# Kernel optimization log

Measured on AMD Instinct MI355X. Metric: run time of the kernel, lower is better.

## Reference

```python
import jax, jax.numpy as jnp
import numpy as np

EMBED_DIM = 2048
NUM_HEADS = 32
NUM_KV_GROUPS = 8
HEAD_DIM = EMBED_DIM // NUM_HEADS  # 64
KV_DIM = HEAD_DIM * NUM_KV_GROUPS  # 512
SCALE = HEAD_DIM ** -0.5


def setup_inputs() -> dict:
    key = jax.random.key(0)
    ks = jax.random.split(key, 11)
    B, T, C = 2, 2048, EMBED_DIM
    s = C ** -0.5
    return {
        "query": jax.random.normal(ks[0], (B, T, C), jnp.float32),
        "key": jax.random.normal(ks[1], (B, T, C), jnp.float32),
        "value": jax.random.normal(ks[2], (B, T, C), jnp.float32),
        "q_w": jax.random.normal(ks[3], (C, C), jnp.float32) * s,
        "q_b": jnp.zeros((C,), jnp.float32),
        "k_w": jax.random.normal(ks[4], (KV_DIM, C), jnp.float32) * s,
        "k_b": jnp.zeros((KV_DIM,), jnp.float32),
        "v_w": jax.random.normal(ks[5], (KV_DIM, C), jnp.float32) * s,
        "v_b": jnp.zeros((KV_DIM,), jnp.float32),
        "o_w": jax.random.normal(ks[6], (C, C), jnp.float32) * s,
        "o_b": jnp.zeros((C,), jnp.float32),
    }


def reference(query, key, value, q_w, q_b, k_w, k_b, v_w, v_b, o_w, o_b):
    B, T, C = query.shape
    n_rep = NUM_HEADS // NUM_KV_GROUPS
    # projections (torch Linear: x @ W.T + b)
    q = (query @ q_w.T + q_b).reshape(B, T, NUM_HEADS, HEAD_DIM)
    k = (key @ k_w.T + k_b).reshape(B, T, NUM_KV_GROUPS, HEAD_DIM)
    v = (value @ v_w.T + v_b).reshape(B, T, NUM_KV_GROUPS, HEAD_DIM)
    # GQA: expand KV groups to match query heads (repeat_interleave on head dim)
    k = jnp.repeat(k, n_rep, axis=2)  # (B, T, H, hd)
    v = jnp.repeat(v, n_rep, axis=2)
    q = jnp.transpose(q, (0, 2, 1, 3)) * SCALE  # (B, H, T, hd)
    k = jnp.transpose(k, (0, 2, 1, 3))
    v = jnp.transpose(v, (0, 2, 1, 3))
    scores = jnp.einsum("bhqd,bhkd->bhqk", q, k)  # (B, H, T, T)
    attn = jax.nn.softmax(scores.astype(jnp.float32), axis=-1).astype(query.dtype)
    out = jnp.einsum("bhqk,bhkd->bhqd", attn, v)  # (B, H, T, hd)
    out = jnp.transpose(out, (0, 2, 1, 3)).reshape(B, T, C)
    return out @ o_w.T + o_b
```

## Files before the change

kernel.cpp:

```cpp
#include <hip/hip_runtime.h>
#include <stdint.h>
#include <stddef.h>

using short8 = __attribute__((ext_vector_type(8))) short;
using short4v = __attribute__((ext_vector_type(4))) short;
using f32x4  = __attribute__((ext_vector_type(4))) float;
using f32x16 = __attribute__((ext_vector_type(16))) float;
using bf16x8 = __attribute__((ext_vector_type(8))) __bf16;

#define DEVI __device__ __forceinline__

DEVI short bf16r(float f) {
  union { float f; uint32_t u; } x; x.f = f;
  uint32_t r = x.u + 0x7FFFu + ((x.u >> 16) & 1u);
  return (short)(r >> 16);
}

DEVI f32x4 mfma16(short8 a, short8 b, f32x4 c) {
  return __builtin_amdgcn_mfma_f32_16x16x32_bf16(
      __builtin_bit_cast(bf16x8, a), __builtin_bit_cast(bf16x8, b), c, 0, 0, 0);
}

DEVI f32x16 mfma32(short8 a, short8 b, f32x16 c) {
  return __builtin_amdgcn_mfma_f32_32x32x16_bf16(
      __builtin_bit_cast(bf16x8, a), __builtin_bit_cast(bf16x8, b), c, 0, 0, 0);
}

DEVI void gload_lds16(const void* g, void* l) {
  __builtin_amdgcn_global_load_lds(
      (const void __attribute__((address_space(1)))*)g,
      (void __attribute__((address_space(3)))*)l,
      16, 0, 0);
}

DEVI float fexp2(float x) {
  float r;
  asm("v_exp_f32 %0, %1" : "=v"(r) : "v"(x));
  return r;
}

DEVI unsigned cvtpk(float a, float b) {
  unsigned r;
  asm("v_cvt_pk_bf16_f32 %0, %1, %2" : "=v"(r) : "v"(a), "v"(b));
  return r;
}

__global__ void k_cvt2(const float* __restrict__ s0, short* __restrict__ d0,
                       const float* __restrict__ s1, short* __restrict__ d1, int n4) {
  const float* s = blockIdx.z ? s1 : s0;
  short* d = blockIdx.z ? d1 : d0;
  int i = blockIdx.x * blockDim.x + threadIdx.x;
  if (i < n4) {
    f32x4 v = reinterpret_cast<const f32x4*>(s)[i];
    short4v o;
    o[0] = bf16r(v[0]); o[1] = bf16r(v[1]); o[2] = bf16r(v[2]); o[3] = bf16r(v[3]);
    reinterpret_cast<short4v*>(d)[i] = o;
  }
}

__global__ void k_cvt(const float* __restrict__ src, short* __restrict__ dst, int n4) {
  int i = blockIdx.x * blockDim.x + threadIdx.x;
  if (i < n4) {
    f32x4 v = reinterpret_cast<const f32x4*>(src)[i];
    short4v o;
    o[0] = bf16r(v[0]); o[1] = bf16r(v[1]); o[2] = bf16r(v[2]); o[3] = bf16r(v[3]);
    reinterpret_cast<short4v*>(dst)[i] = o;
  }
}

template<bool OUT_F32, bool DUAL>
__global__ __launch_bounds__(256) void k_gemm(
    const short* __restrict__ Aw, const short* __restrict__ Bw,
    const float* __restrict__ bias, void* __restrict__ Cp,
    const short* __restrict__ Aw2, const short* __restrict__ Bw2,
    const float* __restrict__ bias2, void* __restrict__ Cp2,
    int M, int N, int K, float alpha)
{
  if constexpr (DUAL) {
    if (blockIdx.z) { Aw = Aw2; Bw = Bw2; bias = bias2; Cp = Cp2; }
  }
  __shared__ short As[2][128 * 64];
  __shared__ short Bs[2][128 * 64];
  const int t = threadIdx.x;
  const int lane = t & 63;
  const int wid = t >> 6;
  const int wr = wid >> 1, wc = wid & 1;
  const int bm = blockIdx.y * 128;
  const int bn = blockIdx.x * 128;

  f32x4 acc[4][4];
  #pragma unroll
  for (int i = 0; i < 4; ++i)
    #pragma unroll
    for (int j = 0; j < 4; ++j) acc[i][j] = f32x4{0.f, 0.f, 0.f, 0.f};

  const int nt = K >> 6;

  auto stage = [&](const short* G, short (&buf)[128 * 64], int k0) {
    #pragma unroll
    for (int i = 0; i < 4; ++i) {
      int lin = t * 16 + i * 4096;
      int a = lin ^ (((lin >> 7) & 7) << 4);
      int row = a >> 7;
      int col = (a & 127) >> 1;
      const short* g = G + (size_t)row * K + k0 + col;
      gload_lds16(g, (char*)(&buf[0]) + (wid << 10) + (i << 12));
    }
  };

  stage(Aw + (size_t)bm * K, As[0], 0);
  stage(Bw + (size_t)bn * K, Bs[0], 0);
  __syncthreads();

  int cur = 0;
  for (int kt = 0; kt < nt; ++kt) {
    const bool pf = (kt + 1 < nt);
    if (pf) {
      stage(Aw + (size_t)bm * K, As[cur ^ 1], (kt + 1) << 6);
      stage(Bw + (size_t)bn * K, Bs[cur ^ 1], (kt + 1) << 6);
    }
    #pragma unroll
    for (int kk = 0; kk < 2; ++kk) {
      const int kb = (kk * 32 + ((lane >> 4) << 3)) << 1;
      short8 af[4], bfr[4];
      #pragma unroll
      for (int i = 0; i < 4; ++i) {
        int row = wr * 64 + i * 16 + (lane & 15);
        int byte = ((row << 7) + kb) ^ ((row & 7) << 4);
        af[i] = *reinterpret_cast<const short8*>((const char*)(&As[cur][0]) + byte);
      }
      #pragma unroll
      for (int j = 0; j < 4; ++j) {
        int row = wc * 64 + j * 16 + (lane & 15);
        int byte = ((row << 7) + kb) ^ ((row & 7) << 4);
        bfr[j] = *reinterpret_cast<const short8*>((const char*)(&Bs[cur][0]) + byte);
      }
      __builtin_amdgcn_s_setprio(1);
      #pragma unroll
      for (int i = 0; i < 4; ++i)
        #pragma unroll
        for (int j = 0; j < 4; ++j)
          acc[i][j] = mfma16(af[i], bfr[j], acc[i][j]);
      __builtin_amdgcn_s_setprio(0);
    }
    __syncthreads();
    cur ^= 1;
  }

  #pragma unroll
  for (int j = 0; j < 4; ++j) {
    int col = bn + wc * 64 + j * 16 + (lane & 15);
    float bv = bias[col];
    #pragma unroll
    for (int i = 0; i < 4; ++i) {
      int row0 = bm + wr * 64 + i * 16 + ((lane >> 4) << 2);
      #pragma unroll
      for (int r = 0; r < 4; ++r) {
        float v = (acc[i][j][r] + bv) * alpha;
        if constexpr (OUT_F32)
          ((float*)Cp)[(size_t)(row0 + r) * N + col] = v;
        else
          ((short*)Cp)[(size_t)(row0 + r) * N + col] = bf16r(v);
      }
    }
  }
}

__global__ __launch_bounds__(512) void k_attn(
    const short* __restrict__ Q, const short* __restrict__ Kg,
    const short* __restrict__ Vg, short* __restrict__ Op)
{
  constexpr int T = 2048;
  constexpr int NT = T / 64;

  const int orig = blockIdx.x;
  const int wgid = (orig & 7) * 64 + (orig >> 3);
  const int bh = wgid >> 3;
  const int qb = wgid & 7;
  const int b = bh >> 5, h = bh & 31;
  const int g = h >> 2;
  const int q0 = qb * 256;

  const int t = threadIdx.x;
  const int lane = t & 63;
  const int wid = t >> 6;
  const int lo = lane & 31;
  const int hi = lane >> 5;

  __shared__ alignas(16) union {
    struct {
      short Kl[2][64 * 64];
      short Vt[2][64 * 72];
    } s;
    short Ol[8][32 * 72];
  } sm;

  const size_t qrow = (size_t)(b * T + q0 + wid * 32 + lo);
  short8 qf[4];
  #pragma unroll
  for (int s = 0; s < 4; ++s)
    qf[s] = *reinterpret_cast<const short8*>(Q + qrow * 2048 + h * 64 + s * 16 + hi * 8);

  f32x16 o0, o1;
  #pragma unroll
  for (int r = 0; r < 16; ++r) { o0[r] = 0.f; o1[r] = 0.f; }
  float m = -10000.f, l = 0.f;

  const short* Kbase = Kg + (size_t)(b * T) * 512 + g * 64;
  const short* Vbase = Vg + (size_t)(b * T) * 512 + g * 64;

  auto stageK = [&](int buf, int k0) {
    int lin = t * 16;
    int a = lin ^ (((lin >> 7) & 7) << 4);
    int row = a >> 7;
    int col = (a & 127) >> 1;
    gload_lds16(Kbase + (size_t)(k0 + row) * 512 + col,
                (char*)(&sm.s.Kl[buf][0]) + (wid << 10));
  };
  short8 vreg;
  auto loadV = [&](int k0) {
    vreg = *reinterpret_cast<const short8*>(
        Vbase + (size_t)(k0 + lane) * 512 + wid * 8);
  };
  auto writeV = [&](int buf) {
    #pragma unroll
    for (int e = 0; e < 8; ++e)
      sm.s.Vt[buf][(wid * 8 + e) * 72 + lane] = vreg[e];
  };

  stageK(0, 0);
  loadV(0);
  writeV(0);
  __syncthreads();

  int cur = 0;
  for (int kt = 0; kt < NT; ++kt) {
    const bool pf = (kt + 1 < NT);
    if (pf) { stageK(cur ^ 1, (kt + 1) * 64); loadV((kt + 1) * 64); }

    short8 kf[2][4];
    #pragma unroll
    for (int tt = 0; tt < 2; ++tt)
      #pragma unroll
      for (int s = 0; s < 4; ++s) {
        int row = tt * 32 + lo;
        int byte = ((row << 7) + (s << 5) + (hi << 4)) ^ ((row & 7) << 4);
        kf[tt][s] = *reinterpret_cast<const short8*>((const char*)(&sm.s.Kl[cur][0]) + byte);
      }
    f32x16 st0, st1;
    #pragma unroll
    for (int r = 0; r < 16; ++r) { st0[r] = 0.f; st1[r] = 0.f; }
    #pragma unroll
    for (int s = 0; s < 4; ++s) {
      st0 = mfma32(kf[0][s], qf[s], st0);
      st1 = mfma32(kf[1][s], qf[s], st1);
    }

    float mx = st0[0];
    #pragma unroll
    for (int r = 1; r < 16; ++r) mx = fmaxf(mx, st0[r]);
    #pragma unroll
    for (int r = 0; r < 16; ++r) mx = fmaxf(mx, st1[r]);
    mx = fmaxf(mx, __shfl_xor(mx, 32));
    if (!__all(mx - m <= 8.0f)) {
      float mn = fmaxf(m, mx);
      float sc = fexp2(m - mn);
      m = mn; l *= sc;
      o0 = o0 * sc; o1 = o1 * sc;
    }
    float ssum = 0.f;
    #pragma unroll
    for (int r = 0; r < 16; ++r) { float e = fexp2(st0[r] - m); st0[r] = e; ssum += e; }
    #pragma unroll
    for (int r = 0; r < 16; ++r) { float e = fexp2(st1[r] - m); st1[r] = e; ssum += e; }
    ssum += __shfl_xor(ssum, 32);
    l += ssum;

    short8 pb[4];
    #pragma unroll
    for (int tt = 0; tt < 2; ++tt) {
      const f32x16& sv = tt ? st1 : st0;
      #pragma unroll
      for (int half = 0; half < 2; ++half) {
        unsigned x1 = cvtpk(sv[half * 8 + 0], sv[half * 8 + 1]);
        unsigned x2 = cvtpk(sv[half * 8 + 2], sv[half * 8 + 3]);
        unsigned x3 = cvtpk(sv[half * 8 + 4], sv[half * 8 + 5]);
        unsigned x4 = cvtpk(sv[half * 8 + 6], sv[half * 8 + 7]);
        unsigned y1 = __shfl_xor(x1, 32);
        unsigned y2 = __shfl_xor(x2, 32);
        unsigned y3 = __shfl_xor(x3, 32);
        unsigned y4 = __shfl_xor(x4, 32);
        union { unsigned u[4]; short8 s8; } p;
        p.u[0] = hi ? y3 : x1;
        p.u[1] = hi ? y4 : x2;
        p.u[2] = hi ? x3 : y1;
        p.u[3] = hi ? x4 : y2;
        pb[tt * 2 + half] = p.s8;
      }
    }

    #pragma unroll
    for (int ks = 0; ks < 4; ++ks) {
      {
        int byte = (lo * 144) + (ks << 5) + (hi << 4);
        short8 va = *reinterpret_cast<const short8*>((const char*)(&sm.s.Vt[cur][0]) + byte);
        o0 = mfma32(va, pb[ks], o0);
      }
      {
        int byte = ((32 + lo) * 144) + (ks << 5) + (hi << 4);
        short8 va = *reinterpret_cast<const short8*>((const char*)(&sm.s.Vt[cur][0]) + byte);
        o1 = mfma32(va, pb[ks], o1);
      }
    }

    if (pf) writeV(cur ^ 1);
    __syncthreads();
    cur ^= 1;
  }

  float inv = 1.0f / l;
  #pragma unroll
  for (int dt = 0; dt < 2; ++dt) {
    const f32x16& ov = dt ? o1 : o0;
    #pragma unroll
    for (int r = 0; r < 16; r += 2) {
      unsigned d2 = cvtpk(ov[r] * inv, ov[r + 1] * inv);
      int dpos = dt * 32 + (r & 3) + 8 * (r >> 2) + 4 * hi;
      *reinterpret_cast<unsigned*>((char*)(&sm.Ol[wid][0]) + (lo * 72 + dpos) * 2) = d2;
    }
  }
  __syncthreads();
  #pragma unroll
  for (int i = 0; i < 4; ++i) {
    int c = hi * 4 + i;
    short8 v = *reinterpret_cast<const short8*>((const char*)(&sm.Ol[wid][0]) + lo * 144 + c * 16);
    *reinterpret_cast<short8*>(Op + qrow * 2048 + h * 64 + c * 8) = v;
  }
}

extern "C" void kernel_launch(void* const* d_in, const int* in_sizes, int n_in,
                              void* d_out, int out_size, void* d_ws, size_t ws_size,
                              hipStream_t stream)
{
  const float* query = (const float*)d_in[0];
  const float* key   = (const float*)d_in[1];
  const float* value = (const float*)d_in[2];
  const float* q_w   = (const float*)d_in[3];
  const float* q_b   = (const float*)d_in[4];
  const float* k_w   = (const float*)d_in[5];
  const float* k_b   = (const float*)d_in[6];
  const float* v_w   = (const float*)d_in[7];
  const float* v_b   = (const float*)d_in[8];
  const float* o_w   = (const float*)d_in[9];
  const float* o_b   = (const float*)d_in[10];
  float* out = (float*)d_out;

  char* ws = (char*)d_ws;
  short* q_wb = (short*)(ws);
  short* k_wb = (short*)(ws + 8388608);
  short* v_wb = (short*)(ws + 10485760);
  short* o_wb = (short*)(ws + 12582912);
  short* R1   = (short*)(ws + 20971520);
  short* R2   = (short*)(ws + 37748736);
  short* Kp   = (short*)(ws + 54525952);
  short* Vp   = (short*)(ws + 58720256);

  const float ALPHA_Q = 0.125f * 1.4426950408889634f;

  k_cvt2<<<dim3(4096, 1, 2), 256, 0, stream>>>(q_w, q_wb, o_w, o_wb, 1048576);
  k_cvt2<<<dim3(1024, 1, 2), 256, 0, stream>>>(k_w, k_wb, v_w, v_wb, 262144);
  k_cvt2<<<dim3(8192, 1, 2), 256, 0, stream>>>(key, R1, value, R2, 2097152);

  k_gemm<false, true><<<dim3(4, 32, 2), 256, 0, stream>>>(
      R1, k_wb, k_b, Kp, R2, v_wb, v_b, Vp, 4096, 512, 2048, 1.0f);

  k_cvt<<<8192, 256, 0, stream>>>(query, R1, 2097152);

  k_gemm<false, false><<<dim3(16, 32), 256, 0, stream>>>(
      R1, q_wb, q_b, R2, nullptr, nullptr, nullptr, nullptr, 4096, 2048, 2048, ALPHA_Q);

  k_attn<<<dim3(512), dim3(512), 0, stream>>>(R2, Kp, Vp, R1);

  k_gemm<true, false><<<dim3(16, 32), 256, 0, stream>>>(
      R1, o_wb, o_b, out, nullptr, nullptr, nullptr, nullptr, 4096, 2048, 2048, 1.0f);
}
```

Measured before the change: 257.6 us.

## Software-pipeline attention loop: overlap next QK^T with current PV, triple-buffer V

After: 263.1 us. 2.1% more time.

```diff
diff --git a/kernel.cpp b/kernel.cpp
--- a/kernel.cpp
+++ b/kernel.cpp
@@ -166,7 +166,7 @@
   }
 }
 
-__global__ __launch_bounds__(512) void k_attn(
+__global__ __launch_bounds__(512, 4) void k_attn(
     const short* __restrict__ Q, const short* __restrict__ Kg,
     const short* __restrict__ Vg, short* __restrict__ Op)
 {
@@ -190,7 +190,7 @@
   __shared__ alignas(16) union {
     struct {
       short Kl[2][64 * 64];
-      short Vt[2][64 * 72];
+      short Vt[3][64 * 72];
     } s;
     short Ol[8][32 * 72];
   } sm;
@@ -228,34 +228,38 @@
       sm.s.Vt[buf][(wid * 8 + e) * 72 + lane] = vreg[e];
   };
 
-  stageK(0, 0);
-  loadV(0);
-  writeV(0);
-  __syncthreads();
-
-  int cur = 0;
-  for (int kt = 0; kt < NT; ++kt) {
-    const bool pf = (kt + 1 < NT);
-    if (pf) { stageK(cur ^ 1, (kt + 1) * 64); loadV((kt + 1) * 64); }
-
-    short8 kf[2][4];
-    #pragma unroll
-    for (int tt = 0; tt < 2; ++tt)
+  f32x16 st0, st1;
+  short8 pb[4];
+
+  auto qkt = [&](int kbuf) {
+    const char* base = (const char*)(&sm.s.Kl[kbuf][0]);
+    #pragma unroll
+    for (int r = 0; r < 16; ++r) { st0[r] = 0.f; st1[r] = 0.f; }
+    {
+      short8 kf[4];
       #pragma unroll
       for (int s = 0; s < 4; ++s) {
-        int row = tt * 32 + lo;
+        int row = lo;
         int byte = ((row << 7) + (s << 5) + (hi << 4)) ^ ((row & 7) << 4);
-        kf[tt][s] = *reinterpret_cast<const short8*>((const char*)(&sm.s.Kl[cur][0]) + byte);
-      }
-    f32x16 st0, st1;
-    #pragma unroll
-    for (int r = 0; r < 16; ++r) { st0[r] = 0.f; st1[r] = 0.f; }
-    #pragma unroll
-    for (int s = 0; s < 4; ++s) {
-      st0 = mfma32(kf[0][s], qf[s], st0);
-      st1 = mfma32(kf[1][s], qf[s], st1);
-    }
-
+        kf[s] = *reinterpret_cast<const short8*>(base + byte);
+      }
+      #pragma unroll
+      for (int s = 0; s < 4; ++s) st0 = mfma32(kf[s], qf[s], st0);
+    }
+    {
+      short8 kf[4];
+      #pragma unroll
+      for (int s = 0; s < 4; ++s) {
+        int row = 32 + lo;
+        int byte = ((row << 7) + (s << 5) + (hi << 4)) ^ ((row & 7) << 4);
+        kf[s] = *reinterpret_cast<const short8*>(base + byte);
+      }
+      #pragma unroll
+      for (int s = 0; s < 4; ++s) st1 = mfma32(kf[s], qf[s], st1);
+    }
+  };
+
+  auto softmax_pack = [&]() {
     float mx = st0[0];
     #pragma unroll
     for (int r = 1; r < 16; ++r) mx = fmaxf(mx, st0[r]);
@@ -276,7 +280,6 @@
     ssum += __shfl_xor(ssum, 32);
     l += ssum;
 
-    short8 pb[4];
     #pragma unroll
     for (int tt = 0; tt < 2; ++tt) {
       const f32x16& sv = tt ? st1 : st0;
@@ -298,25 +301,48 @@
         pb[tt * 2 + half] = p.s8;
       }
     }
-
+  };
+
+  auto pv = [&](int vbuf) {
+    const char* base = (const char*)(&sm.s.Vt[vbuf][0]);
     #pragma unroll
     for (int ks = 0; ks < 4; ++ks) {
       {
         int byte = (lo * 144) + (ks << 5) + (hi << 4);
-        short8 va = *reinterpret_cast<const short8*>((const char*)(&sm.s.Vt[cur][0]) + byte);
+        short8 va = *reinterpret_cast<const short8*>(base + byte);
         o0 = mfma32(va, pb[ks], o0);
       }
       {
         int byte = ((32 + lo) * 144) + (ks << 5) + (hi << 4);
-        short8 va = *reinterpret_cast<const short8*>((const char*)(&sm.s.Vt[cur][0]) + byte);
+        short8 va = *reinterpret_cast<const short8*>(base + byte);
         o1 = mfma32(va, pb[ks], o1);
       }
     }
-
-    if (pf) writeV(cur ^ 1);
+  };
+
+  stageK(0, 0); loadV(0); writeV(0);
+  __syncthreads();
+  qkt(0);
+  stageK(1, 64); loadV(64);
+  softmax_pack();
+  writeV(1);
+  __syncthreads();
+  qkt(1);
+
+  int rb = 0, wb = 2;
+  for (int kt = 1; kt < NT; ++kt) {
+    const bool pf = (kt + 1 < NT);
+    if (pf) { stageK((kt + 1) & 1, (kt + 1) * 64); loadV((kt + 1) * 64); }
+    pv(rb);
+    softmax_pack();
+    if (pf) writeV(wb);
     __syncthreads();
-    cur ^= 1;
-  }
+    if (pf) qkt((kt + 1) & 1);
+    rb = (rb == 2) ? 0 : rb + 1;
+    wb = (wb == 2) ? 0 : wb + 1;
+  }
+  pv(rb);
+  __syncthreads();
 
   float inv = 1.0f / l;
   #pragma unroll
```
